# Performance work log

Measured on AMD Instinct MI355X. Metric: run time of the kernel, lower is better.

The kernel has to match this reference:

```python
import jax, jax.numpy as jnp
import numpy as np

MARGIN = 1.0  # RankLoss(margin=1)


def _rank_loss(emb, labels):
    """pytorch-metric-learning: TripletMarginMiner(semihard) + TripletMarginLoss
    with LpDistance (normalize_embeddings=True, p=2) and ThresholdReducer(low=0).
    emb: [B, D] float, labels: [B] float.
    """
    B = emb.shape[0]
    # LpDistance normalizes embeddings by default
    e = emb / jnp.clip(jnp.linalg.norm(emb, axis=-1, keepdims=True), 1e-12)
    sq = jnp.sum(e * e, axis=-1)                      # [B]
    d2 = sq[:, None] + sq[None, :] - 2.0 * (e @ e.T)  # [B, B]
    dist = jnp.sqrt(jnp.maximum(d2, 0.0))             # pairwise L2

    same = labels[:, None] == labels[None, :]
    eye = jnp.eye(B, dtype=bool)
    pos = same & ~eye          # valid anchor-positive pairs
    neg = ~same                # valid anchor-negative pairs

    ap = dist[:, :, None]      # [B(a), B(p), 1]
    an = dist[:, None, :]      # [B(a), 1, B(n)]
    valid = pos[:, :, None] & neg[:, None, :]          # [B, B, B]
    tm = an - ap               # triplet_margin (LpDistance not inverted)
    # semihard: 0 < an - ap <= margin   (mining is under no_grad -> bool masks)
    mined = valid & (tm > 0.0) & (tm <= MARGIN)

    loss_v = jnp.maximum(ap - an + MARGIN, 0.0)        # TripletMarginLoss per-triplet
    keep = mined & (loss_v > 0.0)                      # ThresholdReducer(low=0)
    cnt = jnp.sum(keep)
    total = jnp.sum(jnp.where(keep, loss_v, 0.0))
    return jnp.where(cnt > 0, total / jnp.maximum(cnt, 1).astype(loss_v.dtype), 0.0)


def setup_inputs() -> dict:
    key = jax.random.key(0)
    k1, k2, k3, k4, k5 = jax.random.split(key, 5)
    N, B, S, D = 3, 384, 25, 128
    return {
        "input": jax.random.normal(k1, (N, B, S), jnp.float32),
        "vr_classes": jax.random.normal(k2, (N, B, D), jnp.float32),
        "target": jax.random.normal(k3, (B, S, N), jnp.float32),
        "target_class": jax.random.randint(k4, (B, 2), 0, 10, jnp.int32),
        "label_item": jax.random.randint(k5, (B,), 0, 8, jnp.int32),
        "optimizers_idx": -1,
    }


def reference(input, vr_classes, target, target_class, label_item, optimizers_idx):
    # optimizers_idx == -1 path: all branches active, loss_sum = sum of branch losses
    labels_f = label_item.astype(jnp.float32)  # raise_range labels (constant)
    n = input.shape[0]
    losses = []
    for i in range(n):  # small fixed structural loop (3 output heads)
        if i == 2:
            lab = jnp.mean(target[:, :, i], axis=-1)  # target_item_mean as labels
        else:
            lab = labels_f
        losses.append(_rank_loss(vr_classes[i], lab))
    corr_loss_combine = jnp.stack(losses)
    ce_loss = jnp.float32(0.0)
    value_diff_loss = jnp.float32(0.0)
    loss_sum = jnp.sum(corr_loss_combine) + ce_loss + value_diff_loss
    return loss_sum, corr_loss_combine
```

## Files before the change

### kernel.cpp

```cpp
#include <hip/hip_runtime.h>

#define BB 384
#define DD 128
#define NI 3
#define SS 25
#define APB 4
#define BPI (BB / APB)
#define GRID (NI * BPI)
#define PSTRIDE 128

__global__ __launch_bounds__(384) void triplet_kernel(
    const float* __restrict__ vr,
    const float* __restrict__ target,
    const int*   __restrict__ label_item,
    float* __restrict__ part_T,
    int*   __restrict__ part_C)
{
    const int blk  = blockIdx.x;
    const int i    = blk / BPI;
    const int b    = blk % BPI;
    const int a0   = b * APB;
    const int t    = threadIdx.x;
    const int lane = t & 63;
    const int wid  = t >> 6;

    __shared__ float ax[APB][DD];
    __shared__ float aas[APB];
    __shared__ float dp_seg[APB][BB];
    __shared__ int   wp[6][APB];
    __shared__ float labs2[BB];
    __shared__ float rf[6];
    __shared__ int   ri[6];

    if (t < APB * DD / 4) {
        const int k = t >> 5, c = t & 31;
        ((float4*)ax[k])[c] =
            ((const float4*)(vr + ((size_t)i * BB + a0 + k) * DD))[c];
    }

    bool isPos[APB], isNeg[APB];
    if (i < 2) {
        const int li_t = label_item[t];
        #pragma unroll
        for (int k = 0; k < APB; ++k) {
            const int li_a = label_item[a0 + k];
            isPos[k] = (li_t == li_a) && (t != a0 + k);
            isNeg[k] = (li_t != li_a);
        }
    } else {
        float m = 0.0f;
        const float* tp = target + (size_t)t * (SS * NI) + 2;
        #pragma unroll
        for (int s = 0; s < SS; ++s) m += tp[s * NI];
        m *= (1.0f / (float)SS);
        labs2[t] = m;
        __syncthreads();
        #pragma unroll
        for (int k = 0; k < APB; ++k) {
            const float la = labs2[a0 + k];
            isPos[k] = (m == la) && (t != a0 + k);
            isNeg[k] = (m != la);
        }
    }

    int rp[APB];
    const unsigned long long lowmask =
        (lane == 0) ? 0ull : (~0ull >> (64 - lane));
    #pragma unroll
    for (int k = 0; k < APB; ++k) {
        const unsigned long long mpk = __ballot(isPos[k]);
        rp[k] = __popcll(mpk & lowmask);
        if (lane == 0) wp[wid][k] = __popcll(mpk);
    }
    __syncthreads();

    int Pany = 0;
    #pragma unroll
    for (int k = 0; k < APB; ++k) {
        #pragma unroll
        for (int w = 0; w < 6; ++w) Pany += wp[w][k];
    }
    if (Pany == 0) {
        if (t == 0) { part_T[i * PSTRIDE + b] = 0.0f; part_C[i * PSTRIDE + b] = 0; }
        return;
    }

    const float4* xb = (const float4*)(vr + ((size_t)i * BB + t) * DD);
    float ab0 = 0.0f, ab1 = 0.0f, ab2 = 0.0f, ab3 = 0.0f, bb = 0.0f;
    #pragma unroll 4
    for (int c = 0; c < DD / 4; ++c) {
        const float4 bv  = xb[c];
        const float4 a0v = ((const float4*)ax[0])[c];
        const float4 a1v = ((const float4*)ax[1])[c];
        const float4 a2v = ((const float4*)ax[2])[c];
        const float4 a3v = ((const float4*)ax[3])[c];
        ab0 = fmaf(a0v.x, bv.x, ab0); ab0 = fmaf(a0v.y, bv.y, ab0);
        ab0 = fmaf(a0v.z, bv.z, ab0); ab0 = fmaf(a0v.w, bv.w, ab0);
        ab1 = fmaf(a1v.x, bv.x, ab1); ab1 = fmaf(a1v.y, bv.y, ab1);
        ab1 = fmaf(a1v.z, bv.z, ab1); ab1 = fmaf(a1v.w, bv.w, ab1);
        ab2 = fmaf(a2v.x, bv.x, ab2); ab2 = fmaf(a2v.y, bv.y, ab2);
        ab2 = fmaf(a2v.z, bv.z, ab2); ab2 = fmaf(a2v.w, bv.w, ab2);
        ab3 = fmaf(a3v.x, bv.x, ab3); ab3 = fmaf(a3v.y, bv.y, ab3);
        ab3 = fmaf(a3v.z, bv.z, ab3); ab3 = fmaf(a3v.w, bv.w, ab3);
        bb  = fmaf(bv.x,  bv.x, bb ); bb  = fmaf(bv.y,  bv.y, bb );
        bb  = fmaf(bv.z,  bv.z, bb ); bb  = fmaf(bv.w,  bv.w, bb );
    }
    if (t >= a0 && t < a0 + APB) aas[t - a0] = bb;
    __syncthreads();

    const float invb   = 1.0f / fmaxf(sqrtf(bb), 1e-12f);
    const float bbterm = bb * invb * invb;
    const float ab[APB] = { ab0, ab1, ab2, ab3 };
    float d[APB];
    #pragma unroll
    for (int k = 0; k < APB; ++k) {
        const float aak  = aas[k];
        const float inva = 1.0f / fmaxf(sqrtf(aak), 1e-12f);
        const float d2   = aak * inva * inva + bbterm
                           - 2.0f * ab[k] * inva * invb;
        d[k] = sqrtf(fmaxf(d2, 0.0f));
        if (isPos[k]) dp_seg[k][(wid << 6) + rp[k]] = d[k];
    }
    __syncthreads();

    float tot = 0.0f;
    int   cnt = 0;
    #pragma unroll
    for (int k = 0; k < APB; ++k) {
        if (isNeg[k]) {
            const float dk = d[k];
            #pragma unroll
            for (int w = 0; w < 6; ++w) {
                const int    Pw  = wp[w][k];
                const float* seg = &dp_seg[k][w << 6];
                #pragma unroll 4
                for (int p = 0; p < Pw; ++p) {
                    const float term = 1.0f - (dk - seg[p]);
                    if (term > 0.0f && term < 1.0f) { cnt += 1; tot += term; }
                }
            }
        }
    }
    #pragma unroll
    for (int off = 32; off > 0; off >>= 1) {
        tot += __shfl_down(tot, off, 64);
        cnt += __shfl_down(cnt, off, 64);
    }
    if (lane == 0) { rf[wid] = tot; ri[wid] = cnt; }
    __syncthreads();
    if (t == 0) {
        float T = 0.0f; int C = 0;
        #pragma unroll
        for (int w = 0; w < 6; ++w) { T += rf[w]; C += ri[w]; }
        part_T[i * PSTRIDE + b] = T;
        part_C[i * PSTRIDE + b] = C;
    }
}

__global__ __launch_bounds__(384) void finalize_kernel(
    const float* __restrict__ part_T,
    const int*   __restrict__ part_C,
    float* __restrict__ out)
{
    const int t    = threadIdx.x;
    const int lane = t & 63;
    const int wid  = t >> 6;
    const int i    = t >> 7;
    const int b    = t & 127;
    __shared__ float rf[6];
    __shared__ int   ri[6];

    float T = (b < BPI) ? part_T[i * PSTRIDE + b] : 0.0f;
    int   C = (b < BPI) ? part_C[i * PSTRIDE + b] : 0;
    #pragma unroll
    for (int off = 32; off > 0; off >>= 1) {
        T += __shfl_down(T, off, 64);
        C += __shfl_down(C, off, 64);
    }
    if (lane == 0) { rf[wid] = T; ri[wid] = C; }
    __syncthreads();
    if (t == 0) {
        float lsum = 0.0f;
        #pragma unroll
        for (int ii = 0; ii < NI; ++ii) {
            const float Ti = rf[2 * ii] + rf[2 * ii + 1];
            const int   Ci = ri[2 * ii] + ri[2 * ii + 1];
            const float li = (Ci > 0) ? (Ti / (float)Ci) : 0.0f;
            out[1 + ii] = li;
            lsum += li;
        }
        out[0] = lsum;
    }
}

extern "C" void kernel_launch(void* const* d_in, const int* in_sizes, int n_in,
                              void* d_out, int out_size, void* d_ws, size_t ws_size,
                              hipStream_t stream) {
    const float* vr         = (const float*)d_in[1];
    const float* target     = (const float*)d_in[2];
    const int*   label_item = (const int*)d_in[4];
    float* out = (float*)d_out;

    float* part_T = (float*)d_ws;
    int*   part_C = (int*)(part_T + NI * PSTRIDE);

    triplet_kernel<<<GRID, 384, 0, stream>>>(vr, target, label_item,
                                             part_T, part_C);
    finalize_kernel<<<1, 384, 0, stream>>>(part_T, part_C, out);
}
```

Measured before the change: 25.39 us.

## Fuse triplet and finalize kernels via cooperative grid sync, double anchors per block

Merges the two-kernel pipeline into one cooperative launch that uses a grid-wide sync before block 0 reduces the partial sums, removing the second kernel launch. It also raises anchors per block from 4 to 8, which halves the grid to 144 blocks and amortizes each candidate row load over more anchors. The cost is grid-sync overhead, cooperative-launch overhead, and more serial work per block in the mining loop, which already varies in length from block to block.

```diff
diff --git a/kernel.cpp b/kernel.cpp
--- a/kernel.cpp
+++ b/kernel.cpp
@@ -1,20 +1,24 @@
 #include <hip/hip_runtime.h>
+#include <hip/hip_cooperative_groups.h>
+
+namespace cg = cooperative_groups;
 
 #define BB 384
 #define DD 128
 #define NI 3
 #define SS 25
-#define APB 4
+#define APB 8
 #define BPI (BB / APB)
 #define GRID (NI * BPI)
-#define PSTRIDE 128
-
-__global__ __launch_bounds__(384) void triplet_kernel(
+#define PSTRIDE 64
+
+__global__ __launch_bounds__(384) void fused_kernel(
     const float* __restrict__ vr,
     const float* __restrict__ target,
     const int*   __restrict__ label_item,
     float* __restrict__ part_T,
-    int*   __restrict__ part_C)
+    int*   __restrict__ part_C,
+    float* __restrict__ out)
 {
     const int blk  = blockIdx.x;
     const int i    = blk / BPI;
@@ -24,7 +28,7 @@
     const int lane = t & 63;
     const int wid  = t >> 6;
 
-    __shared__ float ax[APB][DD];
+    __shared__ float ax[APB * DD];
     __shared__ float aas[APB];
     __shared__ float dp_seg[APB][BB];
     __shared__ int   wp[6][APB];
@@ -32,11 +36,9 @@
     __shared__ float rf[6];
     __shared__ int   ri[6];
 
-    if (t < APB * DD / 4) {
-        const int k = t >> 5, c = t & 31;
-        ((float4*)ax[k])[c] =
-            ((const float4*)(vr + ((size_t)i * BB + a0 + k) * DD))[c];
-    }
+    if (t < APB * DD / 4)
+        ((float4*)ax)[t] =
+            ((const float4*)(vr + ((size_t)i * BB + a0) * DD))[t];
 
     bool isPos[APB], isNeg[APB];
     if (i < 2) {
@@ -80,116 +82,106 @@
         #pragma unroll
         for (int w = 0; w < 6; ++w) Pany += wp[w][k];
     }
-    if (Pany == 0) {
-        if (t == 0) { part_T[i * PSTRIDE + b] = 0.0f; part_C[i * PSTRIDE + b] = 0; }
-        return;
-    }
-
-    const float4* xb = (const float4*)(vr + ((size_t)i * BB + t) * DD);
-    float ab0 = 0.0f, ab1 = 0.0f, ab2 = 0.0f, ab3 = 0.0f, bb = 0.0f;
-    #pragma unroll 4
-    for (int c = 0; c < DD / 4; ++c) {
-        const float4 bv  = xb[c];
-        const float4 a0v = ((const float4*)ax[0])[c];
-        const float4 a1v = ((const float4*)ax[1])[c];
-        const float4 a2v = ((const float4*)ax[2])[c];
-        const float4 a3v = ((const float4*)ax[3])[c];
-        ab0 = fmaf(a0v.x, bv.x, ab0); ab0 = fmaf(a0v.y, bv.y, ab0);
-        ab0 = fmaf(a0v.z, bv.z, ab0); ab0 = fmaf(a0v.w, bv.w, ab0);
-        ab1 = fmaf(a1v.x, bv.x, ab1); ab1 = fmaf(a1v.y, bv.y, ab1);
-        ab1 = fmaf(a1v.z, bv.z, ab1); ab1 = fmaf(a1v.w, bv.w, ab1);
-        ab2 = fmaf(a2v.x, bv.x, ab2); ab2 = fmaf(a2v.y, bv.y, ab2);
-        ab2 = fmaf(a2v.z, bv.z, ab2); ab2 = fmaf(a2v.w, bv.w, ab2);
-        ab3 = fmaf(a3v.x, bv.x, ab3); ab3 = fmaf(a3v.y, bv.y, ab3);
-        ab3 = fmaf(a3v.z, bv.z, ab3); ab3 = fmaf(a3v.w, bv.w, ab3);
-        bb  = fmaf(bv.x,  bv.x, bb ); bb  = fmaf(bv.y,  bv.y, bb );
-        bb  = fmaf(bv.z,  bv.z, bb ); bb  = fmaf(bv.w,  bv.w, bb );
-    }
-    if (t >= a0 && t < a0 + APB) aas[t - a0] = bb;
-    __syncthreads();
-
-    const float invb   = 1.0f / fmaxf(sqrtf(bb), 1e-12f);
-    const float bbterm = bb * invb * invb;
-    const float ab[APB] = { ab0, ab1, ab2, ab3 };
-    float d[APB];
-    #pragma unroll
-    for (int k = 0; k < APB; ++k) {
-        const float aak  = aas[k];
-        const float inva = 1.0f / fmaxf(sqrtf(aak), 1e-12f);
-        const float d2   = aak * inva * inva + bbterm
-                           - 2.0f * ab[k] * inva * invb;
-        d[k] = sqrtf(fmaxf(d2, 0.0f));
-        if (isPos[k]) dp_seg[k][(wid << 6) + rp[k]] = d[k];
-    }
-    __syncthreads();
-
-    float tot = 0.0f;
-    int   cnt = 0;
-    #pragma unroll
-    for (int k = 0; k < APB; ++k) {
-        if (isNeg[k]) {
-            const float dk = d[k];
+
+    if (Pany > 0) {
+        const float4* xb = (const float4*)(vr + ((size_t)i * BB + t) * DD);
+        float ab[APB];
+        #pragma unroll
+        for (int k = 0; k < APB; ++k) ab[k] = 0.0f;
+        float bb = 0.0f;
+        for (int c = 0; c < DD / 4; ++c) {
+            const float4 bv = xb[c];
+            bb = fmaf(bv.x, bv.x, bb); bb = fmaf(bv.y, bv.y, bb);
+            bb = fmaf(bv.z, bv.z, bb); bb = fmaf(bv.w, bv.w, bb);
             #pragma unroll
-            for (int w = 0; w < 6; ++w) {
-                const int    Pw  = wp[w][k];
-                const float* seg = &dp_seg[k][w << 6];
-                #pragma unroll 4
-                for (int p = 0; p < Pw; ++p) {
-                    const float term = 1.0f - (dk - seg[p]);
-                    if (term > 0.0f && term < 1.0f) { cnt += 1; tot += term; }
+            for (int k = 0; k < APB; ++k) {
+                const float4 av = ((const float4*)(ax + k * DD))[c];
+                ab[k] = fmaf(av.x, bv.x, ab[k]);
+                ab[k] = fmaf(av.y, bv.y, ab[k]);
+                ab[k] = fmaf(av.z, bv.z, ab[k]);
+                ab[k] = fmaf(av.w, bv.w, ab[k]);
+            }
+        }
+        if (t >= a0 && t < a0 + APB) aas[t - a0] = bb;
+        __syncthreads();
+
+        const float invb   = 1.0f / fmaxf(sqrtf(bb), 1e-12f);
+        const float bbterm = bb * invb * invb;
+        float d[APB];
+        #pragma unroll
+        for (int k = 0; k < APB; ++k) {
+            const float aak  = aas[k];
+            const float inva = 1.0f / fmaxf(sqrtf(aak), 1e-12f);
+            const float d2   = aak * inva * inva + bbterm
+                               - 2.0f * ab[k] * inva * invb;
+            d[k] = sqrtf(fmaxf(d2, 0.0f));
+            if (isPos[k]) dp_seg[k][(wid << 6) + rp[k]] = d[k];
+        }
+        __syncthreads();
+
+        float tot = 0.0f;
+        int   cnt = 0;
+        #pragma unroll
+        for (int k = 0; k < APB; ++k) {
+            if (isNeg[k]) {
+                const float dk = d[k];
+                #pragma unroll
+                for (int w = 0; w < 6; ++w) {
+                    const int    Pw  = wp[w][k];
+                    const float* seg = &dp_seg[k][w << 6];
+                    #pragma unroll 4
+                    for (int p = 0; p < Pw; ++p) {
+                        const float term = 1.0f - (dk - seg[p]);
+                        if (term > 0.0f && term < 1.0f) { cnt += 1; tot += term; }
+                    }
                 }
             }
         }
-    }
-    #pragma unroll
-    for (int off = 32; off > 0; off >>= 1) {
-        tot += __shfl_down(tot, off, 64);
-        cnt += __shfl_down(cnt, off, 64);
-    }
-    if (lane == 0) { rf[wid] = tot; ri[wid] = cnt; }
-    __syncthreads();
-    if (t == 0) {
-        float T = 0.0f; int C = 0;
-        #pragma unroll
-        for (int w = 0; w < 6; ++w) { T += rf[w]; C += ri[w]; }
-        part_T[i * PSTRIDE + b] = T;
-        part_C[i * PSTRIDE + b] = C;
-    }
-}
-
-__global__ __launch_bounds__(384) void finalize_kernel(
-    const float* __restrict__ part_T,
-    const int*   __restrict__ part_C,
-    float* __restrict__ out)
-{
-    const int t    = threadIdx.x;
-    const int lane = t & 63;
-    const int wid  = t >> 6;
-    const int i    = t >> 7;
-    const int b    = t & 127;
-    __shared__ float rf[6];
-    __shared__ int   ri[6];
-
-    float T = (b < BPI) ? part_T[i * PSTRIDE + b] : 0.0f;
-    int   C = (b < BPI) ? part_C[i * PSTRIDE + b] : 0;
-    #pragma unroll
-    for (int off = 32; off > 0; off >>= 1) {
-        T += __shfl_down(T, off, 64);
-        C += __shfl_down(C, off, 64);
-    }
-    if (lane == 0) { rf[wid] = T; ri[wid] = C; }
-    __syncthreads();
-    if (t == 0) {
-        float lsum = 0.0f;
-        #pragma unroll
-        for (int ii = 0; ii < NI; ++ii) {
-            const float Ti = rf[2 * ii] + rf[2 * ii + 1];
-            const int   Ci = ri[2 * ii] + ri[2 * ii + 1];
-            const float li = (Ci > 0) ? (Ti / (float)Ci) : 0.0f;
-            out[1 + ii] = li;
-            lsum += li;
-        }
-        out[0] = lsum;
+        #pragma unroll
+        for (int off = 32; off > 0; off >>= 1) {
+            tot += __shfl_down(tot, off, 64);
+            cnt += __shfl_down(cnt, off, 64);
+        }
+        if (lane == 0) { rf[wid] = tot; ri[wid] = cnt; }
+        __syncthreads();
+        if (t == 0) {
+            float T = 0.0f; int C = 0;
+            #pragma unroll
+            for (int w = 0; w < 6; ++w) { T += rf[w]; C += ri[w]; }
+            part_T[i * PSTRIDE + b] = T;
+            part_C[i * PSTRIDE + b] = C;
+        }
+    } else {
+        if (t == 0) { part_T[i * PSTRIDE + b] = 0.0f; part_C[i * PSTRIDE + b] = 0; }
+    }
+
+    cg::this_grid().sync();
+
+    if (blk == 0) {
+        const int ii = t >> 7;
+        const int bb2 = t & 127;
+        float T = (bb2 < BPI) ? part_T[ii * PSTRIDE + bb2] : 0.0f;
+        int   C = (bb2 < BPI) ? part_C[ii * PSTRIDE + bb2] : 0;
+        #pragma unroll
+        for (int off = 32; off > 0; off >>= 1) {
+            T += __shfl_down(T, off, 64);
+            C += __shfl_down(C, off, 64);
+        }
+        __syncthreads();
+        if (lane == 0) { rf[wid] = T; ri[wid] = C; }
+        __syncthreads();
+        if (t == 0) {
+            float lsum = 0.0f;
+            #pragma unroll
+            for (int j = 0; j < NI; ++j) {
+                const float Tj = rf[2 * j] + rf[2 * j + 1];
+                const int   Cj = ri[2 * j] + ri[2 * j + 1];
+                const float lj = (Cj > 0) ? (Tj / (float)Cj) : 0.0f;
+                out[1 + j] = lj;
+                lsum += lj;
+            }
+            out[0] = lsum;
+        }
     }
 }
 
@@ -204,7 +196,8 @@
     float* part_T = (float*)d_ws;
     int*   part_C = (int*)(part_T + NI * PSTRIDE);
 
-    triplet_kernel<<<GRID, 384, 0, stream>>>(vr, target, label_item,
-                                             part_T, part_C);
-    finalize_kernel<<<1, 384, 0, stream>>>(part_T, part_C, out);
+    void* args[] = { (void*)&vr, (void*)&target, (void*)&label_item,
+                     (void*)&part_T, (void*)&part_C, (void*)&out };
+    hipLaunchCooperativeKernel((const void*)fused_kernel,
+                               dim3(GRID), dim3(384), args, 0, stream);
 }
```

Measured after the change: 70.60 us. 178% more time.
